# Performance work log

Hardware: AMD Instinct MI355X
Metric: run time of the kernel (lower is better)

The kernel has to match this reference:

```python
import jax, jax.numpy as jnp
import numpy as np

B, S, HID = 1, 2048, 2048
H, HK, D, DV = 16, 4, 128, 128
ROPE = 64  # head_dim * partial_rotary_factor
SCALE = D ** -0.5


def _rotate_half(x):
    x1, x2 = x[..., : x.shape[-1] // 2], x[..., x.shape[-1] // 2:]
    return jnp.concatenate((-x2, x1), axis=-1)


def setup_inputs() -> dict:
    key = jax.random.key(0)
    ks = jax.random.split(key, 6)
    hidden_states = jax.random.normal(ks[0], (B, S, HID), dtype=jnp.float32)
    # real RoPE tables: positions x inv_freq over rope_dim, HF half-duplicated layout
    inv_freq = 1.0 / (10000.0 ** (jnp.arange(0, ROPE, 2, dtype=jnp.float32) / ROPE))
    ang = jnp.arange(S, dtype=jnp.float32)[:, None] * inv_freq[None, :]  # [S, ROPE/2]
    ang = jnp.concatenate([ang, ang], axis=-1)  # [S, ROPE]
    cos = jnp.broadcast_to(jnp.cos(ang)[None], (B, S, ROPE))
    sin = jnp.broadcast_to(jnp.sin(ang)[None], (B, S, ROPE))
    Wq = jax.random.normal(ks[1], (HID, H * D), dtype=jnp.float32) * 0.02
    Wk = jax.random.normal(ks[2], (HID, HK * D), dtype=jnp.float32) * 0.02
    Wv = jax.random.normal(ks[3], (HID, HK * DV), dtype=jnp.float32) * 0.02
    Wo = jax.random.normal(ks[4], (H * DV, HID), dtype=jnp.float32) * 0.02
    sink = jax.random.normal(ks[5], (H,), dtype=jnp.float32)
    return {"hidden_states": hidden_states, "cos": cos, "sin": sin,
            "Wq": Wq, "Wk": Wk, "Wv": Wv, "Wo": Wo, "sink": sink}


def reference(hidden_states, cos, sin, Wq, Wk, Wv, Wo, sink):
    b, s, _ = hidden_states.shape
    q = (hidden_states @ Wq).reshape(b, s, H, D).transpose(0, 2, 1, 3)    # [B,H,S,D]
    k = (hidden_states @ Wk).reshape(b, s, HK, D).transpose(0, 2, 1, 3)   # [B,HK,S,D]
    v = (hidden_states @ Wv).reshape(b, s, HK, DV).transpose(0, 2, 1, 3)  # [B,HK,S,DV]
    # partial RoPE on the first ROPE dims
    c = cos[:, None, :, :]  # [B,1,S,ROPE]
    sn = sin[:, None, :, :]
    q_r, q_n = q[..., :ROPE], q[..., ROPE:]
    k_r, k_n = k[..., :ROPE], k[..., ROPE:]
    q_r = q_r * c + _rotate_half(q_r) * sn
    k_r = k_r * c + _rotate_half(k_r) * sn
    q = jnp.concatenate([q_r, q_n], axis=-1)
    k = jnp.concatenate([k_r, k_n], axis=-1)
    # GQA: repeat kv heads
    g = H // HK
    k = jnp.broadcast_to(k[:, :, None], (b, HK, g, s, D)).reshape(b, H, s, D)
    v = jnp.broadcast_to(v[:, :, None], (b, HK, g, s, DV)).reshape(b, H, s, DV)
    scores = jnp.einsum("bhqd,bhkd->bhqk", q, k) * SCALE
    causal = jnp.triu(jnp.ones((s, s), dtype=bool), k=1)
    scores = jnp.where(causal[None, None], -jnp.inf, scores)
    # sink-bias softmax: sink logit joins the normalizer but gets no value
    m = jnp.max(scores, axis=-1, keepdims=True)                      # [B,H,S,1]
    sink_exp = jnp.exp(sink.reshape(1, H, 1, 1) - m)
    attn_exp = jnp.exp(scores - m)
    attn = attn_exp / (jnp.sum(attn_exp, axis=-1, keepdims=True) + sink_exp)
    out = jnp.einsum("bhqk,bhkv->bhqv", attn, v)                     # [B,H,S,DV]
    out = out.transpose(0, 2, 1, 3).reshape(b, s, H * DV)
    return out @ Wo
```

## Files before the change

### kernel.cpp

```cpp
#include <hip/hip_runtime.h>

#define S_LEN 2048
#define HID_D 2048
#define NH 16
#define NHK 4
#define HD 128
#define ATT_SCALE 0.08838834764831845f
#define NEG_INF (-3.0e38f)

typedef __attribute__((ext_vector_type(8))) __bf16 bf16x8;
typedef __attribute__((ext_vector_type(4))) __bf16 bf16x4;
typedef __attribute__((ext_vector_type(4))) float f32x4;

__global__ __launch_bounds__(256) void f32_to_bf16_kernel(
    const float* __restrict__ in, __bf16* __restrict__ out, int n4) {
  int i = blockIdx.x * 256 + threadIdx.x;
  if (i < n4) {
    float4 v = *reinterpret_cast<const float4*>(&in[(size_t)i * 4]);
    bf16x4 o;
    o[0] = (__bf16)v.x; o[1] = (__bf16)v.y; o[2] = (__bf16)v.z; o[3] = (__bf16)v.w;
    *reinterpret_cast<bf16x4*>(&out[(size_t)i * 4]) = o;
  }
}

__global__ __launch_bounds__(256) void transpose_f32_to_bf16(
    const float* __restrict__ W, __bf16* __restrict__ WT, int K, int N) {
  __shared__ float Ts[64][68];
  const int t = threadIdx.x;
  const int bk = blockIdx.y * 64, bn = blockIdx.x * 64;
  const int r = t >> 4, c4 = (t & 15) << 2;
#pragma unroll
  for (int i = 0; i < 4; ++i) {
    float4 v = *reinterpret_cast<const float4*>(
        &W[(size_t)(bk + r + 16 * i) * N + bn + c4]);
    *reinterpret_cast<float4*>(&Ts[r + 16 * i][c4]) = v;
  }
  __syncthreads();
#pragma unroll
  for (int i = 0; i < 4; ++i) {
    int n_l = r + 16 * i;
    bf16x4 o;
#pragma unroll
    for (int j = 0; j < 4; ++j) o[j] = (__bf16)Ts[c4 + j][n_l];
    *reinterpret_cast<bf16x4*>(&WT[(size_t)(bn + n_l) * K + bk + c4]) = o;
  }
}

__device__ __forceinline__ void gload_lds16(const void* g, void* l) {
  __builtin_amdgcn_global_load_lds(
      (__attribute__((address_space(1))) void*)g,
      (__attribute__((address_space(3))) void*)l, 16, 0, 0);
}

__device__ __forceinline__ void mfma_gemm_tile(
    const __bf16* __restrict__ A, const __bf16* __restrict__ BT,
    float* __restrict__ C, int N, int K, int bm, int bn) {
  __shared__ __attribute__((aligned(16))) __bf16 As[128 * 64];
  __shared__ __attribute__((aligned(16))) __bf16 Bs[128 * 64];
  const int tid = threadIdx.x;
  const int wave = tid >> 6, lane = tid & 63;
  const int wr = (wave >> 1) * 64, wc = (wave & 1) * 64;
  const int l16 = lane & 15, lhi = lane >> 4;

  f32x4 acc[4][4];
#pragma unroll
  for (int i = 0; i < 4; ++i)
#pragma unroll
    for (int j = 0; j < 4; ++j) acc[i][j] = (f32x4){0.f, 0.f, 0.f, 0.f};

  const __bf16* Abase = A + (size_t)bm * K;
  const __bf16* Bbase = BT + (size_t)bn * K;

  for (int k0 = 0; k0 < K; k0 += 64) {
#pragma unroll
    for (int it = 0; it < 4; ++it) {
      int base = it * 256 + wave * 64;
      int f = base + lane;
      int row = f >> 3, ch = f & 7;
      gload_lds16(Abase + (size_t)row * K + k0 + ch * 8, As + base * 8);
      gload_lds16(Bbase + (size_t)row * K + k0 + ch * 8, Bs + base * 8);
    }
    __syncthreads();

#pragma unroll
    for (int kk = 0; kk < 2; ++kk) {
      bf16x8 af[4], bfr[4];
#pragma unroll
      for (int i = 0; i < 4; ++i) {
        af[i] = *reinterpret_cast<const bf16x8*>(
            As + (wr + i * 16 + l16) * 64 + kk * 32 + lhi * 8);
        bfr[i] = *reinterpret_cast<const bf16x8*>(
            Bs + (wc + i * 16 + l16) * 64 + kk * 32 + lhi * 8);
      }
#pragma unroll
      for (int i = 0; i < 4; ++i)
#pragma unroll
        for (int j = 0; j < 4; ++j)
          acc[i][j] = __builtin_amdgcn_mfma_f32_16x16x32_bf16(
              af[i], bfr[j], acc[i][j], 0, 0, 0);
    }
    __syncthreads();
  }

#pragma unroll
  for (int i = 0; i < 4; ++i)
#pragma unroll
    for (int j = 0; j < 4; ++j) {
#pragma unroll
      for (int r = 0; r < 4; ++r) {
        int row = bm + wr + i * 16 + lhi * 4 + r;
        int col = bn + wc + j * 16 + l16;
        C[(size_t)row * N + col] = acc[i][j][r];
      }
    }
}

__global__ __launch_bounds__(256) void qkv_gemm_kernel(
    const __bf16* __restrict__ hsb, const __bf16* __restrict__ WqT,
    const __bf16* __restrict__ WkT, const __bf16* __restrict__ WvT,
    float* __restrict__ Qb, float* __restrict__ Kb, float* __restrict__ Vb) {
  const int bx = blockIdx.x;
  const int bm = blockIdx.y * 128;
  const __bf16* BT;
  float* Cp;
  int N, bn;
  if (bx < 16)      { BT = WqT; Cp = Qb; N = 2048; bn = bx * 128; }
  else if (bx < 20) { BT = WkT; Cp = Kb; N = 512;  bn = (bx - 16) * 128; }
  else              { BT = WvT; Cp = Vb; N = 512;  bn = (bx - 20) * 128; }
  mfma_gemm_tile(hsb, BT, Cp, N, HID_D, bm, bn);
}

__global__ __launch_bounds__(256) void out_proj_kernel(
    const __bf16* __restrict__ Obf, const __bf16* __restrict__ WoT,
    float* __restrict__ out) {
  mfma_gemm_tile(Obf, WoT, out, HID_D, NH * HD, blockIdx.y * 128,
                 blockIdx.x * 128);
}

__global__ __launch_bounds__(256) void rope_pack_kernel(
    const float* __restrict__ Qb, const float* __restrict__ Kb,
    const float* __restrict__ cs, const float* __restrict__ sn,
    __bf16* __restrict__ Qbf, __bf16* __restrict__ Kbf) {
  const int idx = blockIdx.x * 256 + threadIdx.x;
  const int QE = S_LEN * HID_D;
  int e4 = idx * 4;
  const float* src;
  __bf16* dst;
  int s, col;
  if (e4 < QE) {
    s = e4 >> 11; col = e4 & 2047;
    src = Qb + (size_t)s * 2048; dst = Qbf + (size_t)s * 2048;
  } else {
    e4 -= QE;
    if (e4 >= S_LEN * 512) return;
    s = e4 >> 9; col = e4 & 511;
    src = Kb + (size_t)s * 512; dst = Kbf + (size_t)s * 512;
  }
  float4 v = *reinterpret_cast<const float4*>(&src[col]);
  int hc = col & 127;
  float o[4] = {v.x, v.y, v.z, v.w};
  if (hc < 64) {
    if (hc < 32) {
      float4 p = *reinterpret_cast<const float4*>(&src[col + 32]);
      float pp[4] = {p.x, p.y, p.z, p.w};
#pragma unroll
      for (int t = 0; t < 4; ++t) {
        int i = hc + t;
        o[t] = o[t] * cs[s * 64 + i] - pp[t] * sn[s * 64 + i];
      }
    } else {
      float4 p = *reinterpret_cast<const float4*>(&src[col - 32]);
      float pp[4] = {p.x, p.y, p.z, p.w};
#pragma unroll
      for (int t = 0; t < 4; ++t) {
        int i = hc + t;
        o[t] = o[t] * cs[s * 64 + i] + pp[t] * sn[s * 64 + i];
      }
    }
  }
  bf16x4 ob;
#pragma unroll
  for (int t = 0; t < 4; ++t) ob[t] = (__bf16)o[t];
  *reinterpret_cast<bf16x4*>(&dst[col]) = ob;
}

__device__ __forceinline__ unsigned pack2_bf16(float a, float b) {
  unsigned short lo = __builtin_bit_cast(unsigned short, (__bf16)a);
  unsigned short hi = __builtin_bit_cast(unsigned short, (__bf16)b);
  return (unsigned)lo | ((unsigned)hi << 16);
}

__global__ __launch_bounds__(256, 2) void attn_mfma_kernel(
    const __bf16* __restrict__ Qbf, const __bf16* __restrict__ Kbf,
    const __bf16* __restrict__ Vtb, const float* __restrict__ sink,
    __bf16* __restrict__ Obf) {
  __shared__ __attribute__((aligned(16))) __bf16 Ks[64 * 128];
  __shared__ __attribute__((aligned(16))) __bf16 Vs[128 * 64];

  const int tid = threadIdx.x;
  const int wave = tid >> 6, lane = tid & 63;
  const int l16 = lane & 15, lhi = lane >> 4;
  const int h = blockIdx.y;
  const int hk = h >> 2;
  const int qt = (h < 8) ? (31 - (int)blockIdx.x) : (int)blockIdx.x;
  const int q0 = qt * 64;
  const int qrow = q0 + wave * 16 + l16;

  bf16x8 qf[4];
  {
    const __bf16* qp = Qbf + (size_t)qrow * (NH * HD) + h * HD + lhi * 8;
#pragma unroll
    for (int d = 0; d < 4; ++d)
      qf[d] = *reinterpret_cast<const bf16x8*>(qp + d * 32);
  }

  float m = NEG_INF, l_ = 0.f;
  f32x4 acc[8];
#pragma unroll
  for (int f = 0; f < 8; ++f) acc[f] = (f32x4){0.f, 0.f, 0.f, 0.f};

  const int xs7 = l16 & 7;
  const int nt = qt + 1;
  for (int kt = 0; kt < nt; ++kt) {
#pragma unroll
    for (int it = 0; it < 4; ++it) {
      int base = it * 256 + wave * 64;
      int f = base + lane;
      {
        int row = f >> 4, ch = f & 15;
        int sch = (ch & 8) | ((ch ^ row) & 7);
        gload_lds16(Kbf + (size_t)(kt * 64 + row) * (NHK * HD) + hk * HD +
                        sch * 8,
                    Ks + base * 8);
      }
      {
        int dv = f >> 3, ch = f & 7;
        int sch = (ch ^ dv) & 7;
        gload_lds16(Vtb + (size_t)(hk * HD + dv) * S_LEN + kt * 64 + sch * 8,
                    Vs + base * 8);
      }
    }
    __syncthreads();

    f32x4 sc[4];
#pragma unroll
    for (int kb = 0; kb < 4; ++kb) sc[kb] = (f32x4){0.f, 0.f, 0.f, 0.f};
#pragma unroll
    for (int d = 0; d < 4; ++d) {
#pragma unroll
      for (int kb = 0; kb < 4; ++kb) {
        int row = kb * 16 + l16;
        int ch = (d * 4 + lhi) ^ xs7;
        bf16x8 kf = *reinterpret_cast<const bf16x8*>(Ks + row * 128 + ch * 8);
        sc[kb] = __builtin_amdgcn_mfma_f32_16x16x32_bf16(kf, qf[d], sc[kb],
                                                         0, 0, 0);
      }
    }

    float s[4][4];
    const bool last = (kt == qt);
#pragma unroll
    for (int kb = 0; kb < 4; ++kb)
#pragma unroll
      for (int r = 0; r < 4; ++r) {
        float sv = sc[kb][r] * ATT_SCALE;
        if (last) {
          int kc = kt * 64 + kb * 16 + lhi * 4 + r;
          if (kc > qrow) sv = NEG_INF;
        }
        s[kb][r] = sv;
      }
    float tmax = s[0][0];
#pragma unroll
    for (int kb = 0; kb < 4; ++kb)
#pragma unroll
      for (int r = 0; r < 4; ++r) tmax = fmaxf(tmax, s[kb][r]);
    tmax = fmaxf(tmax, __shfl_xor(tmax, 16));
    tmax = fmaxf(tmax, __shfl_xor(tmax, 32));
    float mn = fmaxf(m, tmax);
    float fac = __expf(m - mn);
    m = mn;
    float p[4][4];
    float rs = 0.f;
#pragma unroll
    for (int kb = 0; kb < 4; ++kb)
#pragma unroll
      for (int r = 0; r < 4; ++r) {
        float pv = __expf(s[kb][r] - mn);
        p[kb][r] = pv;
        rs += pv;
      }
    rs += __shfl_xor(rs, 16);
    rs += __shfl_xor(rs, 32);
    l_ = l_ * fac + rs;

    float facb[4];
#pragma unroll
    for (int r = 0; r < 4; ++r) facb[r] = __shfl(fac, lhi * 4 + r);
#pragma unroll
    for (int f = 0; f < 8; ++f)
#pragma unroll
      for (int r = 0; r < 4; ++r) acc[f][r] *= facb[r];

    unsigned pk[4][2];
#pragma unroll
    for (int kb = 0; kb < 4; ++kb) {
      pk[kb][0] = pack2_bf16(p[kb][0], p[kb][1]);
      pk[kb][1] = pack2_bf16(p[kb][2], p[kb][3]);
    }
    const int s0 = l16 + 16 * (2 * (lhi & 1));
    const int s1 = s0 + 16;
    const bool hihalf = (lhi >= 2);
    bf16x8 pa[2];
#pragma unroll
    for (int c = 0; c < 2; ++c) {
      unsigned aw0 = __shfl((int)pk[2 * c][0], s0);
      unsigned aw1 = __shfl((int)pk[2 * c][1], s0);
      unsigned aw2 = __shfl((int)pk[2 * c][0], s1);
      unsigned aw3 = __shfl((int)pk[2 * c][1], s1);
      unsigned bw0 = __shfl((int)pk[2 * c + 1][0], s0);
      unsigned bw1 = __shfl((int)pk[2 * c + 1][1], s0);
      unsigned bw2 = __shfl((int)pk[2 * c + 1][0], s1);
      unsigned bw3 = __shfl((int)pk[2 * c + 1][1], s1);
      uint4 w;
      w.x = hihalf ? bw0 : aw0;
      w.y = hihalf ? bw1 : aw1;
      w.z = hihalf ? bw2 : aw2;
      w.w = hihalf ? bw3 : aw3;
      pa[c] = __builtin_bit_cast(bf16x8, w);
    }

#pragma unroll
    for (int c = 0; c < 2; ++c) {
#pragma unroll
      for (int dvf = 0; dvf < 8; ++dvf) {
        int row = dvf * 16 + l16;
        int ch = (c * 4 + lhi) ^ xs7;
        bf16x8 vf = *reinterpret_cast<const bf16x8*>(Vs + row * 64 + ch * 8);
        acc[dvf] = __builtin_amdgcn_mfma_f32_16x16x32_bf16(pa[c], vf, acc[dvf],
                                                           0, 0, 0);
      }
    }
    __syncthreads();
  }

  float inv = 1.0f / (l_ + __expf(sink[h] - m));
  float invb[4];
#pragma unroll
  for (int r = 0; r < 4; ++r) invb[r] = __shfl(inv, lhi * 4 + r);
#pragma unroll
  for (int dvf = 0; dvf < 8; ++dvf)
#pragma unroll
    for (int r = 0; r < 4; ++r) {
      int row = q0 + wave * 16 + lhi * 4 + r;
      Obf[(size_t)row * (NH * HD) + h * HD + dvf * 16 + l16] =
          (__bf16)(acc[dvf][r] * invb[r]);
    }
}

extern "C" void kernel_launch(void* const* d_in, const int* in_sizes, int n_in,
                              void* d_out, int out_size, void* d_ws,
                              size_t ws_size, hipStream_t stream) {
  const float* hs   = (const float*)d_in[0];
  const float* cosb = (const float*)d_in[1];
  const float* sinb = (const float*)d_in[2];
  const float* Wq   = (const float*)d_in[3];
  const float* Wk   = (const float*)d_in[4];
  const float* Wv   = (const float*)d_in[5];
  const float* Wo   = (const float*)d_in[6];
  const float* sink = (const float*)d_in[7];
  float* out = (float*)d_out;

  float* Qb = (float*)d_ws;
  float* Kb = Qb + (size_t)S_LEN * (NH * HD);
  float* Vb = Kb + (size_t)S_LEN * (NHK * HD);
  __bf16* hsb = (__bf16*)(Vb + (size_t)S_LEN * (NHK * HD));
  __bf16* WqT = hsb + (size_t)S_LEN * HID_D;
  __bf16* WkT = WqT + (size_t)HID_D * (NH * HD);
  __bf16* WvT = WkT + (size_t)HID_D * (NHK * HD);
  __bf16* WoT = WvT + (size_t)HID_D * (NHK * HD);
  __bf16* Qbf = hsb;
  __bf16* Kbf = WkT;
  __bf16* Vtb = WvT;
  __bf16* Obf = WqT;

  f32_to_bf16_kernel<<<dim3(4096), 256, 0, stream>>>(hs, hsb,
                                                     S_LEN * HID_D / 4);
  transpose_f32_to_bf16<<<dim3(32, 32), 256, 0, stream>>>(Wq, WqT, HID_D, 2048);
  transpose_f32_to_bf16<<<dim3(8, 32), 256, 0, stream>>>(Wk, WkT, HID_D, 512);
  transpose_f32_to_bf16<<<dim3(8, 32), 256, 0, stream>>>(Wv, WvT, HID_D, 512);
  transpose_f32_to_bf16<<<dim3(32, 32), 256, 0, stream>>>(Wo, WoT, 2048, 2048);

  qkv_gemm_kernel<<<dim3(24, 16), 256, 0, stream>>>(hsb, WqT, WkT, WvT,
                                                    Qb, Kb, Vb);

  rope_pack_kernel<<<dim3(5120), 256, 0, stream>>>(Qb, Kb, cosb, sinb,
                                                   Qbf, Kbf);
  transpose_f32_to_bf16<<<dim3(8, 32), 256, 0, stream>>>(Vb, Vtb, S_LEN, 512);

  attn_mfma_kernel<<<dim3(32, 16), 256, 0, stream>>>(Qbf, Kbf, Vtb, sink, Obf);
  out_proj_kernel<<<dim3(16, 16), 256, 0, stream>>>(Obf, WoT, out);
}
```

Measured before the change: 277.2 us.

## Merge prep kernels, fuse RoPE/V-transpose into QKV GEMM epilogue, double-buffer LDS

```diff
diff --git a/kernel.cpp b/kernel.cpp
--- a/kernel.cpp
+++ b/kernel.cpp
@@ -12,51 +12,70 @@
 typedef __attribute__((ext_vector_type(4))) __bf16 bf16x4;
 typedef __attribute__((ext_vector_type(4))) float f32x4;
 
-__global__ __launch_bounds__(256) void f32_to_bf16_kernel(
-    const float* __restrict__ in, __bf16* __restrict__ out, int n4) {
-  int i = blockIdx.x * 256 + threadIdx.x;
-  if (i < n4) {
-    float4 v = *reinterpret_cast<const float4*>(&in[(size_t)i * 4]);
-    bf16x4 o;
-    o[0] = (__bf16)v.x; o[1] = (__bf16)v.y; o[2] = (__bf16)v.z; o[3] = (__bf16)v.w;
-    *reinterpret_cast<bf16x4*>(&out[(size_t)i * 4]) = o;
-  }
-}
-
-__global__ __launch_bounds__(256) void transpose_f32_to_bf16(
-    const float* __restrict__ W, __bf16* __restrict__ WT, int K, int N) {
-  __shared__ float Ts[64][68];
-  const int t = threadIdx.x;
-  const int bk = blockIdx.y * 64, bn = blockIdx.x * 64;
-  const int r = t >> 4, c4 = (t & 15) << 2;
-#pragma unroll
-  for (int i = 0; i < 4; ++i) {
-    float4 v = *reinterpret_cast<const float4*>(
-        &W[(size_t)(bk + r + 16 * i) * N + bn + c4]);
-    *reinterpret_cast<float4*>(&Ts[r + 16 * i][c4]) = v;
-  }
-  __syncthreads();
-#pragma unroll
-  for (int i = 0; i < 4; ++i) {
-    int n_l = r + 16 * i;
-    bf16x4 o;
-#pragma unroll
-    for (int j = 0; j < 4; ++j) o[j] = (__bf16)Ts[c4 + j][n_l];
-    *reinterpret_cast<bf16x4*>(&WT[(size_t)(bn + n_l) * K + bk + c4]) = o;
-  }
-}
-
 __device__ __forceinline__ void gload_lds16(const void* g, void* l) {
   __builtin_amdgcn_global_load_lds(
       (__attribute__((address_space(1))) void*)g,
       (__attribute__((address_space(3))) void*)l, 16, 0, 0);
 }
 
-__device__ __forceinline__ void mfma_gemm_tile(
+__device__ __forceinline__ void transpose_job(
+    const float* __restrict__ W, __bf16* __restrict__ WT, int K, int N,
+    int local, int nbx, float* Ts ) {
+  const int t = threadIdx.x;
+  const int bk = (local / nbx) * 64, bn = (local % nbx) * 64;
+  const int r = t >> 4, c4 = (t & 15) << 2;
+#pragma unroll
+  for (int i = 0; i < 4; ++i) {
+    float4 v = *reinterpret_cast<const float4*>(
+        &W[(size_t)(bk + r + 16 * i) * N + bn + c4]);
+    *reinterpret_cast<float4*>(&Ts[(r + 16 * i) * 68 + c4]) = v;
+  }
+  __syncthreads();
+#pragma unroll
+  for (int i = 0; i < 4; ++i) {
+    int n_l = r + 16 * i;
+    bf16x4 o;
+#pragma unroll
+    for (int j = 0; j < 4; ++j) o[j] = (__bf16)Ts[(c4 + j) * 68 + n_l];
+    *reinterpret_cast<bf16x4*>(&WT[(size_t)(bn + n_l) * K + bk + c4]) = o;
+  }
+}
+
+__global__ __launch_bounds__(256) void prep_kernel(
+    const float* __restrict__ hs, const float* __restrict__ Wq,
+    const float* __restrict__ Wk, const float* __restrict__ Wv,
+    const float* __restrict__ Wo, __bf16* __restrict__ hsb,
+    __bf16* __restrict__ WqT, __bf16* __restrict__ WkT,
+    __bf16* __restrict__ WvT, __bf16* __restrict__ WoT) {
+  __shared__ float Ts[64 * 68];
+  const int b = blockIdx.x;
+  if (b < 4096) {
+    int i = b * 256 + threadIdx.x;
+    if (i < S_LEN * HID_D / 4) {
+      float4 v = *reinterpret_cast<const float4*>(&hs[(size_t)i * 4]);
+      bf16x4 o;
+      o[0] = (__bf16)v.x; o[1] = (__bf16)v.y;
+      o[2] = (__bf16)v.z; o[3] = (__bf16)v.w;
+      *reinterpret_cast<bf16x4*>(&hsb[(size_t)i * 4]) = o;
+    }
+  } else if (b < 5120) {
+    transpose_job(Wq, WqT, 2048, 2048, b - 4096, 32, Ts);
+  } else if (b < 5376) {
+    transpose_job(Wk, WkT, 2048, 512, b - 5120, 8, Ts);
+  } else if (b < 5632) {
+    transpose_job(Wv, WvT, 2048, 512, b - 5376, 8, Ts);
+  } else {
+    transpose_job(Wo, WoT, 2048, 2048, b - 5632, 32, Ts);
+  }
+}
+
+template <int MODE>
+__device__ __forceinline__ void mfma_gemm_tile_db(
+    __bf16* As, __bf16* Bs,
     const __bf16* __restrict__ A, const __bf16* __restrict__ BT,
-    float* __restrict__ C, int N, int K, int bm, int bn) {
-  __shared__ __attribute__((aligned(16))) __bf16 As[128 * 64];
-  __shared__ __attribute__((aligned(16))) __bf16 Bs[128 * 64];
+    float* __restrict__ C, __bf16* __restrict__ Db,
+    const float* __restrict__ cs, const float* __restrict__ sn,
+    int N, int K, int bm, int bn) {
   const int tid = threadIdx.x;
   const int wave = tid >> 6, lane = tid & 63;
   const int wr = (wave >> 1) * 64, wc = (wave & 1) * 64;
@@ -70,27 +89,37 @@
 
   const __bf16* Abase = A + (size_t)bm * K;
   const __bf16* Bbase = BT + (size_t)bn * K;
-
-  for (int k0 = 0; k0 < K; k0 += 64) {
+  const int nk = K >> 6;
+
+  auto stage = [&](int buf, int k0) {
 #pragma unroll
     for (int it = 0; it < 4; ++it) {
       int base = it * 256 + wave * 64;
       int f = base + lane;
       int row = f >> 3, ch = f & 7;
-      gload_lds16(Abase + (size_t)row * K + k0 + ch * 8, As + base * 8);
-      gload_lds16(Bbase + (size_t)row * K + k0 + ch * 8, Bs + base * 8);
-    }
-    __syncthreads();
-
+      gload_lds16(Abase + (size_t)row * K + k0 + ch * 8,
+                  As + buf * 8192 + base * 8);
+      gload_lds16(Bbase + (size_t)row * K + k0 + ch * 8,
+                  Bs + buf * 8192 + base * 8);
+    }
+  };
+
+  stage(0, 0);
+  __syncthreads();
+  for (int t = 0; t < nk; ++t) {
+    const int buf = t & 1;
+    if (t + 1 < nk) stage(buf ^ 1, (t + 1) * 64);
+    const __bf16* Ab = As + buf * 8192;
+    const __bf16* Bb = Bs + buf * 8192;
 #pragma unroll
     for (int kk = 0; kk < 2; ++kk) {
       bf16x8 af[4], bfr[4];
 #pragma unroll
       for (int i = 0; i < 4; ++i) {
         af[i] = *reinterpret_cast<const bf16x8*>(
-            As + (wr + i * 16 + l16) * 64 + kk * 32 + lhi * 8);
+            Ab + (wr + i * 16 + l16) * 64 + kk * 32 + lhi * 8);
         bfr[i] = *reinterpret_cast<const bf16x8*>(
-            Bs + (wc + i * 16 + l16) * 64 + kk * 32 + lhi * 8);
+            Bb + (wc + i * 16 + l16) * 64 + kk * 32 + lhi * 8);
       }
 #pragma unroll
       for (int i = 0; i < 4; ++i)
@@ -102,86 +131,90 @@
     __syncthreads();
   }
 
-#pragma unroll
-  for (int i = 0; i < 4; ++i)
-#pragma unroll
-    for (int j = 0; j < 4; ++j) {
-#pragma unroll
-      for (int r = 0; r < 4; ++r) {
-        int row = bm + wr + i * 16 + lhi * 4 + r;
-        int col = bn + wc + j * 16 + l16;
-        C[(size_t)row * N + col] = acc[i][j][r];
-      }
-    }
-}
-
-__global__ __launch_bounds__(256) void qkv_gemm_kernel(
+  if (MODE == 0) {
+#pragma unroll
+    for (int i = 0; i < 4; ++i)
+#pragma unroll
+      for (int j = 0; j < 4; ++j)
+#pragma unroll
+        for (int r = 0; r < 4; ++r)
+          C[(size_t)(bm + wr + i * 16 + lhi * 4 + r) * N + bn + wc + j * 16 +
+            l16] = acc[i][j][r];
+  } else if (MODE == 3) {
+#pragma unroll
+    for (int i = 0; i < 4; ++i)
+#pragma unroll
+      for (int j = 0; j < 4; ++j) {
+        bf16x4 o;
+#pragma unroll
+        for (int r = 0; r < 4; ++r) o[r] = (__bf16)acc[i][j][r];
+        *reinterpret_cast<bf16x4*>(
+            &Db[(size_t)(bn + wc + j * 16 + l16) * S_LEN + bm + wr + i * 16 +
+                lhi * 4]) = o;
+      }
+  } else {
+    const int dst = (MODE == 1) ? (NH * HD) : (NHK * HD);
+    if (wc == 0) {
+#pragma unroll
+      for (int i = 0; i < 4; ++i)
+#pragma unroll
+        for (int r = 0; r < 4; ++r) {
+          int s = bm + wr + i * 16 + lhi * 4 + r;
+          const float* cp = cs + (size_t)s * 64;
+          const float* sp = sn + (size_t)s * 64;
+          float c0 = cp[l16], c1 = cp[16 + l16];
+          float c2 = cp[32 + l16], c3 = cp[48 + l16];
+          float s0 = sp[l16], s1 = sp[16 + l16];
+          float s2 = sp[32 + l16], s3 = sp[48 + l16];
+          float x0 = acc[i][0][r], x1 = acc[i][1][r];
+          float x2 = acc[i][2][r], x3 = acc[i][3][r];
+          __bf16* dp = Db + (size_t)s * dst + bn;
+          dp[l16]      = (__bf16)(x0 * c0 - x2 * s0);
+          dp[16 + l16] = (__bf16)(x1 * c1 - x3 * s1);
+          dp[32 + l16] = (__bf16)(x2 * c2 + x0 * s2);
+          dp[48 + l16] = (__bf16)(x3 * c3 + x1 * s3);
+        }
+    } else {
+#pragma unroll
+      for (int i = 0; i < 4; ++i)
+#pragma unroll
+        for (int j = 0; j < 4; ++j)
+#pragma unroll
+          for (int r = 0; r < 4; ++r)
+            Db[(size_t)(bm + wr + i * 16 + lhi * 4 + r) * dst + bn + wc +
+               j * 16 + l16] = (__bf16)acc[i][j][r];
+    }
+  }
+}
+
+__global__ __launch_bounds__(256, 2) void qkv_gemm_kernel(
     const __bf16* __restrict__ hsb, const __bf16* __restrict__ WqT,
     const __bf16* __restrict__ WkT, const __bf16* __restrict__ WvT,
-    float* __restrict__ Qb, float* __restrict__ Kb, float* __restrict__ Vb) {
+    __bf16* __restrict__ Qbf, __bf16* __restrict__ Kbf,
+    __bf16* __restrict__ Vtb, const float* __restrict__ cs,
+    const float* __restrict__ sn) {
+  __shared__ __attribute__((aligned(16))) __bf16 As[2 * 8192];
+  __shared__ __attribute__((aligned(16))) __bf16 Bs[2 * 8192];
   const int bx = blockIdx.x;
   const int bm = blockIdx.y * 128;
-  const __bf16* BT;
-  float* Cp;
-  int N, bn;
-  if (bx < 16)      { BT = WqT; Cp = Qb; N = 2048; bn = bx * 128; }
-  else if (bx < 20) { BT = WkT; Cp = Kb; N = 512;  bn = (bx - 16) * 128; }
-  else              { BT = WvT; Cp = Vb; N = 512;  bn = (bx - 20) * 128; }
-  mfma_gemm_tile(hsb, BT, Cp, N, HID_D, bm, bn);
-}
-
-__global__ __launch_bounds__(256) void out_proj_kernel(
+  if (bx < 16)
+    mfma_gemm_tile_db<1>(As, Bs, hsb, WqT, nullptr, Qbf, cs, sn, 2048, HID_D,
+                         bm, bx * 128);
+  else if (bx < 20)
+    mfma_gemm_tile_db<2>(As, Bs, hsb, WkT, nullptr, Kbf, cs, sn, 512, HID_D,
+                         bm, (bx - 16) * 128);
+  else
+    mfma_gemm_tile_db<3>(As, Bs, hsb, WvT, nullptr, Vtb, cs, sn, 512, HID_D,
+                         bm, (bx - 20) * 128);
+}
+
+__global__ __launch_bounds__(256, 2) void out_proj_kernel(
     const __bf16* __restrict__ Obf, const __bf16* __restrict__ WoT,
     float* __restrict__ out) {
-  mfma_gemm_tile(Obf, WoT, out, HID_D, NH * HD, blockIdx.y * 128,
-                 blockIdx.x * 128);
-}
-
-__global__ __launch_bounds__(256) void rope_pack_kernel(
-    const float* __restrict__ Qb, const float* __restrict__ Kb,
-    const float* __restrict__ cs, const float* __restrict__ sn,
-    __bf16* __restrict__ Qbf, __bf16* __restrict__ Kbf) {
-  const int idx = blockIdx.x * 256 + threadIdx.x;
-  const int QE = S_LEN * HID_D;
-  int e4 = idx * 4;
-  const float* src;
-  __bf16* dst;
-  int s, col;
-  if (e4 < QE) {
-    s = e4 >> 11; col = e4 & 2047;
-    src = Qb + (size_t)s * 2048; dst = Qbf + (size_t)s * 2048;
-  } else {
-    e4 -= QE;
-    if (e4 >= S_LEN * 512) return;
-    s = e4 >> 9; col = e4 & 511;
-    src = Kb + (size_t)s * 512; dst = Kbf + (size_t)s * 512;
-  }
-  float4 v = *reinterpret_cast<const float4*>(&src[col]);
-  int hc = col & 127;
-  float o[4] = {v.x, v.y, v.z, v.w};
-  if (hc < 64) {
-    if (hc < 32) {
-      float4 p = *reinterpret_cast<const float4*>(&src[col + 32]);
-      float pp[4] = {p.x, p.y, p.z, p.w};
-#pragma unroll
-      for (int t = 0; t < 4; ++t) {
-        int i = hc + t;
-        o[t] = o[t] * cs[s * 64 + i] - pp[t] * sn[s * 64 + i];
-      }
-    } else {
-      float4 p = *reinterpret_cast<const float4*>(&src[col - 32]);
-      float pp[4] = {p.x, p.y, p.z, p.w};
-#pragma unroll
-      for (int t = 0; t < 4; ++t) {
-        int i = hc + t;
-        o[t] = o[t] * cs[s * 64 + i] + pp[t] * sn[s * 64 + i];
-      }
-    }
-  }
-  bf16x4 ob;
-#pragma unroll
-  for (int t = 0; t < 4; ++t) ob[t] = (__bf16)o[t];
-  *reinterpret_cast<bf16x4*>(&dst[col]) = ob;
+  __shared__ __attribute__((aligned(16))) __bf16 As[2 * 8192];
+  __shared__ __attribute__((aligned(16))) __bf16 Bs[2 * 8192];
+  mfma_gemm_tile_db<0>(As, Bs, Obf, WoT, out, nullptr, nullptr, nullptr,
+                       HID_D, NH * HD, blockIdx.y * 128, blockIdx.x * 128);
 }
 
 __device__ __forceinline__ unsigned pack2_bf16(float a, float b) {
@@ -194,8 +227,8 @@
     const __bf16* __restrict__ Qbf, const __bf16* __restrict__ Kbf,
     const __bf16* __restrict__ Vtb, const float* __restrict__ sink,
     __bf16* __restrict__ Obf) {
-  __shared__ __attribute__((aligned(16))) __bf16 Ks[64 * 128];
-  __shared__ __attribute__((aligned(16))) __bf16 Vs[128 * 64];
+  __shared__ __attribute__((aligned(16))) __bf16 Ks[2 * 64 * 128];
+  __shared__ __attribute__((aligned(16))) __bf16 Vs[2 * 128 * 64];
 
   const int tid = threadIdx.x;
   const int wave = tid >> 6, lane = tid & 63;
@@ -219,9 +252,7 @@
 #pragma unroll
   for (int f = 0; f < 8; ++f) acc[f] = (f32x4){0.f, 0.f, 0.f, 0.f};
 
-  const int xs7 = l16 & 7;
-  const int nt = qt + 1;
-  for (int kt = 0; kt < nt; ++kt) {
+  auto stage_kv = [&](int buf, int kt) {
 #pragma unroll
     for (int it = 0; it < 4; ++it) {
       int base = it * 256 + wave * 64;
@@ -231,16 +262,26 @@
         int sch = (ch & 8) | ((ch ^ row) & 7);
         gload_lds16(Kbf + (size_t)(kt * 64 + row) * (NHK * HD) + hk * HD +
                         sch * 8,
-                    Ks + base * 8);
+                    Ks + buf * 8192 + base * 8);
       }
       {
         int dv = f >> 3, ch = f & 7;
         int sch = (ch ^ dv) & 7;
         gload_lds16(Vtb + (size_t)(hk * HD + dv) * S_LEN + kt * 64 + sch * 8,
-                    Vs + base * 8);
-      }
-    }
-    __syncthreads();
+                    Vs + buf * 8192 + base * 8);
+      }
+    }
+  };
+
+  const int xs7 = l16 & 7;
+  const int nt = qt + 1;
+  stage_kv(0, 0);
+  __syncthreads();
+  for (int kt = 0; kt < nt; ++kt) {
+    const int buf = kt & 1;
+    if (kt + 1 < nt) stage_kv(buf ^ 1, kt + 1);
+    const __bf16* Kb_ = Ks + buf * 8192;
+    const __bf16* Vb_ = Vs + buf * 8192;
 
     f32x4 sc[4];
 #pragma unroll
@@ -251,7 +292,7 @@
       for (int kb = 0; kb < 4; ++kb) {
         int row = kb * 16 + l16;
         int ch = (d * 4 + lhi) ^ xs7;
-        bf16x8 kf = *reinterpret_cast<const bf16x8*>(Ks + row * 128 + ch * 8);
+        bf16x8 kf = *reinterpret_cast<const bf16x8*>(Kb_ + row * 128 + ch * 8);
         sc[kb] = __builtin_amdgcn_mfma_f32_16x16x32_bf16(kf, qf[d], sc[kb],
                                                          0, 0, 0);
       }
@@ -336,12 +377,12 @@
       for (int dvf = 0; dvf < 8; ++dvf) {
         int row = dvf * 16 + l16;
         int ch = (c * 4 + lhi) ^ xs7;
-        bf16x8 vf = *reinterpret_cast<const bf16x8*>(Vs + row * 64 + ch * 8);
+        bf16x8 vf = *reinterpret_cast<const bf16x8*>(Vb_ + row * 64 + ch * 8);
         acc[dvf] = __builtin_amdgcn_mfma_f32_16x16x32_bf16(pa[c], vf, acc[dvf],
                                                            0, 0, 0);
       }
     }
-    __syncthreads();
+    if (kt + 1 < nt) __syncthreads();
   }
 
   float inv = 1.0f / (l_ + __expf(sink[h] - m));
@@ -371,33 +412,20 @@
   const float* sink = (const float*)d_in[7];
   float* out = (float*)d_out;
 
-  float* Qb = (float*)d_ws;
-  float* Kb = Qb + (size_t)S_LEN * (NH * HD);
-  float* Vb = Kb + (size_t)S_LEN * (NHK * HD);
-  __bf16* hsb = (__bf16*)(Vb + (size_t)S_LEN * (NHK * HD));
+  __bf16* hsb = (__bf16*)d_ws;
   __bf16* WqT = hsb + (size_t)S_LEN * HID_D;
   __bf16* WkT = WqT + (size_t)HID_D * (NH * HD);
   __bf16* WvT = WkT + (size_t)HID_D * (NHK * HD);
   __bf16* WoT = WvT + (size_t)HID_D * (NHK * HD);
-  __bf16* Qbf = hsb;
-  __bf16* Kbf = WkT;
-  __bf16* Vtb = WvT;
+  __bf16* Qbf = WoT + (size_t)(NH * HD) * HID_D;
+  __bf16* Kbf = Qbf + (size_t)S_LEN * (NH * HD);
+  __bf16* Vtb = Kbf + (size_t)S_LEN * (NHK * HD);
   __bf16* Obf = WqT;
 
-  f32_to_bf16_kernel<<<dim3(4096), 256, 0, stream>>>(hs, hsb,
-                                                     S_LEN * HID_D / 4);
-  transpose_f32_to_bf16<<<dim3(32, 32), 256, 0, stream>>>(Wq, WqT, HID_D, 2048);
-  transpose_f32_to_bf16<<<dim3(8, 32), 256, 0, stream>>>(Wk, WkT, HID_D, 512);
-  transpose_f32_to_bf16<<<dim3(8, 32), 256, 0, stream>>>(Wv, WvT, HID_D, 512);
-  transpose_f32_to_bf16<<<dim3(32, 32), 256, 0, stream>>>(Wo, WoT, 2048, 2048);
-
-  qkv_gemm_kernel<<<dim3(24, 16), 256, 0, stream>>>(hsb, WqT, WkT, WvT,
-                                                    Qb, Kb, Vb);
-
-  rope_pack_kernel<<<dim3(5120), 256, 0, stream>>>(Qb, Kb, cosb, sinb,
-                                                   Qbf, Kbf);
-  transpose_f32_to_bf16<<<dim3(8, 32), 256, 0, stream>>>(Vb, Vtb, S_LEN, 512);
-
+  prep_kernel<<<dim3(6656), 256, 0, stream>>>(hs, Wq, Wk, Wv, Wo, hsb, WqT,
+                                              WkT, WvT, WoT);
+  qkv_gemm_kernel<<<dim3(24, 16), 256, 0, stream>>>(hsb, WqT, WkT, WvT, Qbf,
+                                                    Kbf, Vtb, cosb, sinb);
   attn_mfma_kernel<<<dim3(32, 16), 256, 0, stream>>>(Qbf, Kbf, Vtb, sink, Obf);
   out_proj_kernel<<<dim3(16, 16), 256, 0, stream>>>(Obf, WoT, out);
 }
```

New measurement: 274.8 us. About the same (-0.9%).
